# Performance work log

Hardware: AMD Instinct MI355X
Metric: run time of the kernel (lower is better)

## Reference

```python
import jax, jax.numpy as jnp
import numpy as np

N, G, E, R = 32768, 2048, 1146880, 3
NIN, GIN, F, OUT = 6, 4, 64, 1


def _w(k, fan_in, fan_out):
    return (jax.random.normal(k, (fan_in, fan_out), jnp.float32) / np.sqrt(fan_in)).astype(jnp.float32)


def setup_inputs() -> dict:
    key = jax.random.key(0)
    ks = jax.random.split(key, 20)
    x = jax.random.normal(ks[0], (N, NIN), jnp.float32)
    u = jax.random.normal(ks[1], (G, GIN), jnp.float32)
    batch = jnp.sort(jax.random.randint(ks[2], (N,), 0, G))
    hyperedge_index = jax.random.randint(ks[3], (R, E), 0, N)
    batch_hyper = jnp.sort(jax.random.randint(ks[4], (E,), 0, G))
    inp = {
        "x": x, "u": u, "batch": batch,
        "hyperedge_index": hyperedge_index, "batch_hyper": batch_hyper, "r": R,
        # mlp_x: (NIN+GIN)->F->F->F
        "W1": _w(ks[5], NIN + GIN, F), "b1": jnp.zeros((F,), jnp.float32),
        "W2": _w(ks[6], F, F), "b2": jnp.zeros((F,), jnp.float32),
        "W3": _w(ks[7], F, F), "b3": jnp.zeros((F,), jnp.float32),
        # weighting matrix [F,F]
        "weight": _w(ks[8], F, F),
        # x_hat: 2F->F->F->OUT
        "V1": _w(ks[9], 2 * F, F), "c1": jnp.zeros((F,), jnp.float32),
        "V2": _w(ks[10], F, F), "c2": jnp.zeros((F,), jnp.float32),
        "V3": _w(ks[11], F, OUT), "c3": jnp.zeros((OUT,), jnp.float32),
    }
    return inp


def _segment_softmax(x, idx, num_segments):
    # torch_geometric-style softmax grouped by idx along dim 0, per feature
    seg_max = jax.ops.segment_max(x, idx, num_segments=num_segments)
    ex = jnp.exp(x - seg_max[idx])
    denom = jax.ops.segment_sum(ex, idx, num_segments=num_segments)
    return ex / denom[idx]


def reference(x, u, batch, hyperedge_index, batch_hyper, r,
              W1, b1, W2, b2, W3, b3, weight, V1, c1, V2, c2, V3, c3):
    # mlp_x on [node_feats || global_feats_of_node's_graph]
    h = jnp.concatenate([x, u[batch]], axis=1)            # [N, NIN+GIN]
    h = jnp.maximum(h @ W1 + b1, 0.0)
    h = jnp.maximum(h @ W2 + b2, 0.0)
    h = h @ W3 + b3                                        # [N, F]

    # hyperedge finding: sum the r member-node embeddings of each hyperedge
    x_hyper = jnp.zeros((hyperedge_index.shape[1], h.shape[1]), h.dtype)
    for i in range(hyperedge_index.shape[0]):              # r is small & fixed
        x_hyper = x_hyper + jnp.take(h, hyperedge_index[i], axis=0)  # [E, F]

    # weighting: segment softmax over hyperedges of the same graph
    coef = _segment_softmax(x_hyper, batch_hyper, G)       # [E, F]
    x_hyper_hat = coef * jnp.maximum(x_hyper @ weight, 0.0)

    # x_hat head
    o = jnp.concatenate([x_hyper, x_hyper_hat], axis=1)    # [E, 2F]
    o = jnp.maximum(o @ V1 + c1, 0.0)
    o = jnp.maximum(o @ V2 + c2, 0.0)
    o = jax.nn.sigmoid(o @ V3 + c3)                        # [E, OUT]
    return (o, batch_hyper)
```

## Files before the change

### kernel.cpp

```cpp
#include <hip/hip_runtime.h>
#include <math.h>

typedef short bf16x8 __attribute__((ext_vector_type(8)));
typedef float f32x4  __attribute__((ext_vector_type(4)));
typedef unsigned short u16;
typedef unsigned int   u32;

#define MFMA16 __builtin_amdgcn_mfma_f32_16x16x32_bf16

__device__ __forceinline__ u16 f2b(float x) {
    union { float f; unsigned u; } v; v.f = x;
    unsigned r = v.u + 0x7fffu + ((v.u >> 16) & 1u);
    return (u16)(r >> 16);
}
__device__ __forceinline__ u16 f2bu(float x) {
    union { float f; unsigned u; } v; v.f = x;
    return (u16)((v.u + 0x8000u) >> 16);
}
__device__ __forceinline__ float b2f(u16 h) {
    union { unsigned u; float f; } v; v.u = ((unsigned)h) << 16;
    return v.f;
}
__device__ __forceinline__ float blo(u32 w) {
    union { u32 u; float f; } v; v.u = w << 16; return v.f;
}
__device__ __forceinline__ float bhi(u32 w) {
    union { u32 u; float f; } v; v.u = w & 0xffff0000u; return v.f;
}
__device__ __forceinline__ u32 add3pack(u32 x, u32 y, u32 z) {
    union { float f; u32 u; } lo, hi;
    lo.f = blo(x) + blo(y) + blo(z);
    hi.f = bhi(x) + bhi(y) + bhi(z);
    return __builtin_amdgcn_perm(hi.u + 0x8000u, lo.u + 0x8000u, 0x07060302u);
}
__device__ __forceinline__ u32 pack2(float lo, float hi) {
    union { float f; u32 u; } a, b;
    a.f = lo; b.f = hi;
    return __builtin_amdgcn_perm(b.u + 0x8000u, a.u + 0x8000u, 0x07060302u);
}

#define LOG2E 1.44269504088896340736f

__global__ __launch_bounds__(256) void prep_mlp_kernel(
    const float* __restrict__ x, const float* __restrict__ u,
    const int* __restrict__ batch,
    const float* __restrict__ W1, const float* __restrict__ b1,
    const float* __restrict__ W2, const float* __restrict__ b2,
    const float* __restrict__ W3, const float* __restrict__ b3,
    u16* __restrict__ hb, int N,
    const float* __restrict__ Wg, const float* __restrict__ V1g,
    const float* __restrict__ V2g, u16* __restrict__ SWZ,
    const int* __restrict__ bh, int E, int G, int* __restrict__ seg_start,
    int SB)
{
    const int b = blockIdx.x, tid = threadIdx.x;
    if (b < 32) {
        int idx = b * 256 + tid;
        int k = idx >> 6, n = idx & 63;
        int s1 = (k < 64) ? k : (64 + (((k - 64) & 15) << 2) + ((k - 64) >> 4));
        int off1 = ((s1 >> 5) * 4 + (n >> 4)) * 512 + (n & 15) * 32 + ((s1 >> 3) & 3) * 8 + (s1 & 7);
        SWZ[4096 + off1] = f2b(V1g[idx]);
        if (idx < 4096) {
            int offw = ((k >> 5) * 4 + (n >> 4)) * 512 + (n & 15) * 32 + ((k >> 3) & 3) * 8 + (k & 7);
            SWZ[offw] = f2b(Wg[idx]);
            int s2 = ((k & 15) << 2) + (k >> 4);
            int off2 = ((s2 >> 5) * 4 + (n >> 4)) * 512 + (n & 15) * 32 + ((s2 >> 3) & 3) * 8 + (s2 & 7);
            SWZ[12288 + off2] = f2b(V2g[idx]);
        }
        return;
    }
    if (b < 32 + SB) {
        int g = (b - 32) * 256 + tid;
        if (g > G) return;
        int lo = 0, hi = E;
        while (lo < hi) {
            int mid = (lo + hi) >> 1;
            if (bh[mid] < g) lo = mid + 1; else hi = mid;
        }
        seg_start[g] = lo;
        return;
    }
    __shared__ float inbuf[16][10];
    __shared__ float h1[16][64];
    __shared__ float h2[16][64];
    const int ni = tid >> 6, f = tid & 63;
    const int base = (b - 32 - SB) * 16;
    int nodes[4];
    #pragma unroll
    for (int s = 0; s < 4; ++s) {
        nodes[s] = min(base + s * 4 + ni, N - 1);
        if (f < 6)       inbuf[s * 4 + ni][f] = x[nodes[s] * 6 + f];
        else if (f < 10) inbuf[s * 4 + ni][f] = u[batch[nodes[s]] * 4 + (f - 6)];
    }
    __syncthreads();
    float acc[4];
    #pragma unroll
    for (int s = 0; s < 4; ++s) acc[s] = b1[f];
    #pragma unroll
    for (int k = 0; k < 10; ++k) {
        float w = W1[k * 64 + f];
        #pragma unroll
        for (int s = 0; s < 4; ++s) acc[s] = fmaf(inbuf[s * 4 + ni][k], w, acc[s]);
    }
    #pragma unroll
    for (int s = 0; s < 4; ++s) h1[s * 4 + ni][f] = fmaxf(acc[s], 0.f);
    __syncthreads();
    #pragma unroll
    for (int s = 0; s < 4; ++s) acc[s] = b2[f];
    #pragma unroll
    for (int k4 = 0; k4 < 16; ++k4) {
        float w0 = W2[(k4 * 4 + 0) * 64 + f];
        float w1 = W2[(k4 * 4 + 1) * 64 + f];
        float w2 = W2[(k4 * 4 + 2) * 64 + f];
        float w3 = W2[(k4 * 4 + 3) * 64 + f];
        #pragma unroll
        for (int s = 0; s < 4; ++s) {
            float4 hv = *(const float4*)&h1[s * 4 + ni][k4 * 4];
            acc[s] = fmaf(hv.x, w0, acc[s]);
            acc[s] = fmaf(hv.y, w1, acc[s]);
            acc[s] = fmaf(hv.z, w2, acc[s]);
            acc[s] = fmaf(hv.w, w3, acc[s]);
        }
    }
    #pragma unroll
    for (int s = 0; s < 4; ++s) h2[s * 4 + ni][f] = fmaxf(acc[s], 0.f);
    __syncthreads();
    #pragma unroll
    for (int s = 0; s < 4; ++s) acc[s] = b3[f];
    #pragma unroll
    for (int k4 = 0; k4 < 16; ++k4) {
        float w0 = W3[(k4 * 4 + 0) * 64 + f];
        float w1 = W3[(k4 * 4 + 1) * 64 + f];
        float w2 = W3[(k4 * 4 + 2) * 64 + f];
        float w3 = W3[(k4 * 4 + 3) * 64 + f];
        #pragma unroll
        for (int s = 0; s < 4; ++s) {
            float4 hv = *(const float4*)&h2[s * 4 + ni][k4 * 4];
            acc[s] = fmaf(hv.x, w0, acc[s]);
            acc[s] = fmaf(hv.y, w1, acc[s]);
            acc[s] = fmaf(hv.z, w2, acc[s]);
            acc[s] = fmaf(hv.w, w3, acc[s]);
        }
    }
    #pragma unroll
    for (int s = 0; s < 4; ++s) hb[nodes[s] * 64 + f] = f2b(acc[s]);
}

__global__ __launch_bounds__(256) void gather_stats_kernel(
    const u16* __restrict__ hb, const int* __restrict__ hidx,
    const int* __restrict__ seg_start,
    u16* __restrict__ Xh, float* __restrict__ Sinv,
    float* __restrict__ out, int E)
{
    __shared__ float ps[4][8][8];
    const int tid = threadIdx.x, lane = tid & 63, wid = tid >> 6;
    const int sub = lane >> 3, cl = lane & 7;
    const int g = blockIdx.x;
    const int e0 = seg_start[g], e1 = seg_start[g + 1];
    if (e1 <= e0) return;
    const int e1m1 = e1 - 1;
    const float gf = (float)g;

    for (int e = e0 + tid; e < e1; e += 256) out[E + e] = gf;

    float s[8] = {0.f, 0.f, 0.f, 0.f, 0.f, 0.f, 0.f, 0.f};
    for (int e = e0 + wid * 8 + sub; e < e1; e += 128) {
        #pragma unroll
        for (int j = 0; j < 4; ++j) {
            int ee = e + j * 32;
            int ec = min(ee, e1m1);
            int i0 = hidx[ec], i1 = hidx[E + ec], i2 = hidx[2 * E + ec];
            uint4 A0 = *(const uint4*)(hb + (size_t)i0 * 64 + cl * 8);
            uint4 A1 = *(const uint4*)(hb + (size_t)i1 * 64 + cl * 8);
            uint4 A2 = *(const uint4*)(hb + (size_t)i2 * 64 + cl * 8);
            u32 w0 = add3pack(A0.x, A1.x, A2.x);
            u32 w1 = add3pack(A0.y, A1.y, A2.y);
            u32 w2 = add3pack(A0.z, A1.z, A2.z);
            u32 w3 = add3pack(A0.w, A1.w, A2.w);
            if (ee < e1) {
                uint4 W; W.x = w0; W.y = w1; W.z = w2; W.w = w3;
                *(uint4*)(Xh + (size_t)ee * 64 + cl * 8) = W;
                s[0] += __expf(blo(w0)); s[1] += __expf(bhi(w0));
                s[2] += __expf(blo(w1)); s[3] += __expf(bhi(w1));
                s[4] += __expf(blo(w2)); s[5] += __expf(bhi(w2));
                s[6] += __expf(blo(w3)); s[7] += __expf(bhi(w3));
            }
        }
    }
    #pragma unroll
    for (int k = 0; k < 8; ++k) {
        s[k] += __shfl_xor(s[k], 8);
        s[k] += __shfl_xor(s[k], 16);
        s[k] += __shfl_xor(s[k], 32);
    }
    if (lane < 8) {
        #pragma unroll
        for (int k = 0; k < 8; ++k) ps[wid][lane][k] = s[k];
    }
    __syncthreads();
    if (tid < 64) {
        int c8 = tid >> 3, cc = tid & 7;
        float S = ps[0][c8][cc] + ps[1][c8][cc] + ps[2][c8][cc] + ps[3][c8][cc];
        Sinv[g * 64 + tid] = 1.f / S;
    }
}

__global__ __launch_bounds__(256, 4) void mfma_seg_kernel(
    const u16* __restrict__ Xh, const int* __restrict__ seg_start,
    const u16* __restrict__ SWZ, const float* __restrict__ Sinv,
    const float* __restrict__ c1g, const float* __restrict__ c2g,
    const float* __restrict__ V3g, const float* __restrict__ c3g,
    float* __restrict__ out, int E)
{
    __shared__ u16 SW[16384];
    __shared__ u16 XT_all[4][16 * 64];

    const int tid = threadIdx.x, lane = tid & 63, wid = tid >> 6;
    const int nl = lane & 15, rq = lane >> 4;
    const int g = blockIdx.x;
    const int e0 = seg_start[g], e1 = seg_start[g + 1];
    const int L = e1 - e0;
    if (L <= 0) return;
    const int e1m1 = e1 - 1;

    {
        const uint4* src = (const uint4*)SWZ;
        uint4* dst = (uint4*)SW;
        for (int i = tid; i < 2048; i += 256) dst[i] = src[i];
    }
    __syncthreads();
    const u16* WB  = SW;
    const u16* V1B = SW + 4096;
    const u16* V2B = SW + 12288;

    bf16x8 I0, I1;
    #pragma unroll
    for (int j = 0; j < 8; ++j) {
        I0[j] = (rq * 8 + j == nl)      ? (short)0x3F80 : (short)0;
        I1[j] = (rq * 8 + j == nl + 16) ? (short)0x3F80 : (short)0;
    }

    float l2d[4], c1v[4], c2v[4], v3v[4];
    #pragma unroll
    for (int nt = 0; nt < 4; ++nt) {
        int col = nt * 16 + nl;
        l2d[nt] = __log2f(Sinv[g * 64 + col]);
        c1v[nt] = c1g[col];
        c2v[nt] = c2g[col];
        v3v[nt] = V3g[col];
    }
    const float c3s = c3g[0];
    u16* XT = XT_all[wid];
    const f32x4 zf = {0.f, 0.f, 0.f, 0.f};

    const int xw_swz = rq << 4;
    const int xr_base = nl * 64;
    const int xr_swz  = (nl & 12) << 2;
    const int xr0 = xr_base + ((rq * 8) ^ xr_swz);
    const int xr1 = xr_base + ((rq * 8 + 32) ^ xr_swz);

    auto loadA = [&](int tt, bf16x8& A0, bf16x8& A1) {
        const u16* xp = Xh + (size_t)min(e0 + tt * 16 + nl, e1m1) * 64 + rq * 8;
        A0 = *(const bf16x8*)(xp);
        A1 = *(const bf16x8*)(xp + 32);
    };

    int t = wid;
    bf16x8 p0 = {}, p1 = {};
    if (t * 16 < L) loadA(t, p0, p1);

    for (; t * 16 < L; t += 8) {
        const int eB1 = e0 + t * 16;
        const int eB2 = eB1 + 64;

        bf16x8 a0 = p0, a1 = p1;
        bf16x8 a2, a3;
        loadA(t + 4, a2, a3);
        if ((t + 8) * 16 < L) loadA(t + 8, p0, p1);

        f32x4 xc1[4], xc2[4];
        xc1[0] = MFMA16(a0, I0, zf, 0, 0, 0);
        xc1[1] = MFMA16(a0, I1, zf, 0, 0, 0);
        xc1[2] = MFMA16(a1, I0, zf, 0, 0, 0);
        xc1[3] = MFMA16(a1, I1, zf, 0, 0, 0);
        xc2[0] = MFMA16(a2, I0, zf, 0, 0, 0);
        xc2[1] = MFMA16(a2, I1, zf, 0, 0, 0);
        xc2[2] = MFMA16(a3, I0, zf, 0, 0, 0);
        xc2[3] = MFMA16(a3, I1, zf, 0, 0, 0);

        f32x4 acc1[4] = {zf, zf, zf, zf}, acc2t[4] = {zf, zf, zf, zf};
        #pragma unroll
        for (int nt = 0; nt < 4; ++nt) {
            bf16x8 b0 = *(const bf16x8*)(WB + (0 * 4 + nt) * 512 + nl * 32 + rq * 8);
            acc1[nt]  = MFMA16(a0, b0, acc1[nt], 0, 0, 0);
            acc2t[nt] = MFMA16(a2, b0, acc2t[nt], 0, 0, 0);
            bf16x8 b1 = *(const bf16x8*)(WB + (1 * 4 + nt) * 512 + nl * 32 + rq * 8);
            acc1[nt]  = MFMA16(a1, b1, acc1[nt], 0, 0, 0);
            acc2t[nt] = MFMA16(a3, b1, acc2t[nt], 0, 0, 0);
        }
        #pragma unroll
        for (int r = 0; r < 4; ++r) {
            float v0 = __builtin_amdgcn_exp2f(fmaf(xc1[0][r], LOG2E, l2d[0])) * fmaxf(acc1[0][r], 0.f);
            float v1 = __builtin_amdgcn_exp2f(fmaf(xc1[1][r], LOG2E, l2d[1])) * fmaxf(acc1[1][r], 0.f);
            float v2 = __builtin_amdgcn_exp2f(fmaf(xc1[2][r], LOG2E, l2d[2])) * fmaxf(acc1[2][r], 0.f);
            float v3 = __builtin_amdgcn_exp2f(fmaf(xc1[3][r], LOG2E, l2d[3])) * fmaxf(acc1[3][r], 0.f);
            uint2 w; w.x = pack2(v0, v1); w.y = pack2(v2, v3);
            *(uint2*)(XT + (rq * 4 + r) * 64 + ((nl * 4) ^ xw_swz)) = w;
        }
        bf16x8 x2a = *(const bf16x8*)(XT + xr0);
        bf16x8 x3a = *(const bf16x8*)(XT + xr1);
        #pragma unroll
        for (int r = 0; r < 4; ++r) {
            float v0 = __builtin_amdgcn_exp2f(fmaf(xc2[0][r], LOG2E, l2d[0])) * fmaxf(acc2t[0][r], 0.f);
            float v1 = __builtin_amdgcn_exp2f(fmaf(xc2[1][r], LOG2E, l2d[1])) * fmaxf(acc2t[1][r], 0.f);
            float v2 = __builtin_amdgcn_exp2f(fmaf(xc2[2][r], LOG2E, l2d[2])) * fmaxf(acc2t[2][r], 0.f);
            float v3 = __builtin_amdgcn_exp2f(fmaf(xc2[3][r], LOG2E, l2d[3])) * fmaxf(acc2t[3][r], 0.f);
            uint2 w; w.x = pack2(v0, v1); w.y = pack2(v2, v3);
            *(uint2*)(XT + (rq * 4 + r) * 64 + ((nl * 4) ^ xw_swz)) = w;
        }
        bf16x8 x2b = *(const bf16x8*)(XT + xr0);
        bf16x8 x3b = *(const bf16x8*)(XT + xr1);

        f32x4 va[4], vb[4];
        #pragma unroll
        for (int nt = 0; nt < 4; ++nt) {
            va[nt][0] = c1v[nt]; va[nt][1] = c1v[nt];
            va[nt][2] = c1v[nt]; va[nt][3] = c1v[nt];
            vb[nt] = va[nt];
        }
        #pragma unroll
        for (int nt = 0; nt < 4; ++nt) {
            bf16x8 b0 = *(const bf16x8*)(V1B + (0 * 4 + nt) * 512 + nl * 32 + rq * 8);
            va[nt] = MFMA16(a0, b0, va[nt], 0, 0, 0);
            vb[nt] = MFMA16(a2, b0, vb[nt], 0, 0, 0);
            bf16x8 b1 = *(const bf16x8*)(V1B + (1 * 4 + nt) * 512 + nl * 32 + rq * 8);
            va[nt] = MFMA16(a1, b1, va[nt], 0, 0, 0);
            vb[nt] = MFMA16(a3, b1, vb[nt], 0, 0, 0);
        }
        #pragma unroll
        for (int nt = 0; nt < 4; ++nt) {
            bf16x8 b2 = *(const bf16x8*)(V1B + (2 * 4 + nt) * 512 + nl * 32 + rq * 8);
            va[nt] = MFMA16(x2a, b2, va[nt], 0, 0, 0);
            vb[nt] = MFMA16(x2b, b2, vb[nt], 0, 0, 0);
            bf16x8 b3 = *(const bf16x8*)(V1B + (3 * 4 + nt) * 512 + nl * 32 + rq * 8);
            va[nt] = MFMA16(x3a, b3, va[nt], 0, 0, 0);
            vb[nt] = MFMA16(x3b, b3, vb[nt], 0, 0, 0);
        }
        #pragma unroll
        for (int r = 0; r < 4; ++r) {
            uint2 w;
            w.x = pack2(fmaxf(va[0][r], 0.f), fmaxf(va[1][r], 0.f));
            w.y = pack2(fmaxf(va[2][r], 0.f), fmaxf(va[3][r], 0.f));
            *(uint2*)(XT + (rq * 4 + r) * 64 + ((nl * 4) ^ xw_swz)) = w;
        }
        bf16x8 o0a = *(const bf16x8*)(XT + xr0);
        bf16x8 o1a = *(const bf16x8*)(XT + xr1);
        #pragma unroll
        for (int r = 0; r < 4; ++r) {
            uint2 w;
            w.x = pack2(fmaxf(vb[0][r], 0.f), fmaxf(vb[1][r], 0.f));
            w.y = pack2(fmaxf(vb[2][r], 0.f), fmaxf(vb[3][r], 0.f));
            *(uint2*)(XT + (rq * 4 + r) * 64 + ((nl * 4) ^ xw_swz)) = w;
        }
        bf16x8 o0b = *(const bf16x8*)(XT + xr0);
        bf16x8 o1b = *(const bf16x8*)(XT + xr1);

        f32x4 wa[4], wb2[4];
        #pragma unroll
        for (int nt = 0; nt < 4; ++nt) {
            wa[nt][0] = c2v[nt]; wa[nt][1] = c2v[nt];
            wa[nt][2] = c2v[nt]; wa[nt][3] = c2v[nt];
            wb2[nt] = wa[nt];
        }
        #pragma unroll
        for (int nt = 0; nt < 4; ++nt) {
            bf16x8 b0 = *(const bf16x8*)(V2B + (0 * 4 + nt) * 512 + nl * 32 + rq * 8);
            wa[nt]  = MFMA16(o0a, b0, wa[nt], 0, 0, 0);
            wb2[nt] = MFMA16(o0b, b0, wb2[nt], 0, 0, 0);
            bf16x8 b1 = *(const bf16x8*)(V2B + (1 * 4 + nt) * 512 + nl * 32 + rq * 8);
            wa[nt]  = MFMA16(o1a, b1, wa[nt], 0, 0, 0);
            wb2[nt] = MFMA16(o1b, b1, wb2[nt], 0, 0, 0);
        }

        float sra[4], srb[4];
        #pragma unroll
        for (int r = 0; r < 4; ++r) {
            float u1 = 0.f, u2 = 0.f;
            #pragma unroll
            for (int nt = 0; nt < 4; ++nt) {
                u1 = fmaf(fmaxf(wa[nt][r],  0.f), v3v[nt], u1);
                u2 = fmaf(fmaxf(wb2[nt][r], 0.f), v3v[nt], u2);
            }
            u1 += __shfl_xor(u1, 1); u2 += __shfl_xor(u2, 1);
            u1 += __shfl_xor(u1, 2); u2 += __shfl_xor(u2, 2);
            u1 += __shfl_xor(u1, 4); u2 += __shfl_xor(u2, 4);
            u1 += __shfl_xor(u1, 8); u2 += __shfl_xor(u2, 8);
            sra[r] = 1.f / (1.f + __expf(-(u1 + c3s)));
            srb[r] = 1.f / (1.f + __expf(-(u2 + c3s)));
        }
        if (nl == 0) {
            const int ra = eB1 + rq * 4;
            if (ra + 3 < e1) {
                *(float4*)(out + ra) = make_float4(sra[0], sra[1], sra[2], sra[3]);
            } else {
                #pragma unroll
                for (int r = 0; r < 4; ++r)
                    if (ra + r < e1) out[ra + r] = sra[r];
            }
            const int rb = eB2 + rq * 4;
            if (rb + 3 < e1) {
                *(float4*)(out + rb) = make_float4(srb[0], srb[1], srb[2], srb[3]);
            } else {
                #pragma unroll
                for (int r = 0; r < 4; ++r)
                    if (rb + r < e1) out[rb + r] = srb[r];
            }
        }
    }
}

extern "C" void kernel_launch(void* const* d_in, const int* in_sizes, int n_in,
                              void* d_out, int out_size, void* d_ws, size_t ws_size,
                              hipStream_t stream) {
    const float* x     = (const float*)d_in[0];
    const float* u     = (const float*)d_in[1];
    const int*   batch = (const int*)  d_in[2];
    const int*   hidx  = (const int*)  d_in[3];
    const int*   bh    = (const int*)  d_in[4];
    const float* W1 = (const float*)d_in[6];
    const float* b1 = (const float*)d_in[7];
    const float* W2 = (const float*)d_in[8];
    const float* b2 = (const float*)d_in[9];
    const float* W3 = (const float*)d_in[10];
    const float* b3 = (const float*)d_in[11];
    const float* Wg = (const float*)d_in[12];
    const float* V1 = (const float*)d_in[13];
    const float* c1 = (const float*)d_in[14];
    const float* V2 = (const float*)d_in[15];
    const float* c2 = (const float*)d_in[16];
    const float* V3 = (const float*)d_in[17];
    const float* c3 = (const float*)d_in[18];

    const int N = in_sizes[0] / 6;
    const int G = in_sizes[1] / 4;
    const int E = in_sizes[4];

    char* ws = (char*)d_ws;
    size_t off = 0;
    u16* hb = (u16*)(ws + off);            off += (size_t)N * 64 * 2;
    int* seg_start = (int*)(ws + off);     off += ((size_t)G + 1) * 4;
    off = (off + 255) & ~(size_t)255;
    u16* SWZ = (u16*)(ws + off);           off += 16384 * 2;
    float* Sinv = (float*)(ws + off);      off += (size_t)G * 64 * 4;
    off = (off + 255) & ~(size_t)255;
    u16* Xh = (u16*)(ws + off);            off += (size_t)E * 64 * 2;
    float* out = (float*)d_out;

    const int SB = (G + 256) / 256;
    const int NB = (N + 15) / 16;
    prep_mlp_kernel<<<32 + SB + NB, 256, 0, stream>>>(
        x, u, batch, W1, b1, W2, b2, W3, b3, hb, N,
        Wg, V1, V2, SWZ, bh, E, G, seg_start, SB);
    gather_stats_kernel<<<G, 256, 0, stream>>>(hb, hidx, seg_start, Xh, Sinv, out, E);
    mfma_seg_kernel<<<G, 256, 0, stream>>>(
        Xh, seg_start, SWZ, Sinv, c1, c2, V3, c3, out, E);
}
```

Before: 244.3 us.

## Recompute hyperedge sums in MFMA kernel instead of materializing Xh

Removes the E×64 bf16 intermediate buffer Xh that the stats kernel wrote and the MFMA kernel read back. The MFMA kernel now regathers the three member-node rows from hb (which is small and likely cache-resident) and sums them inline. This saves about 147MB of write plus read traffic at the cost of a second random gather, extra index loads and higher register pressure. Occupancy in launch bounds is lowered from 4 to 3 to make room for those registers.

```diff
diff --git a/kernel.cpp b/kernel.cpp
--- a/kernel.cpp
+++ b/kernel.cpp
@@ -149,8 +149,7 @@
 __global__ __launch_bounds__(256) void gather_stats_kernel(
     const u16* __restrict__ hb, const int* __restrict__ hidx,
     const int* __restrict__ seg_start,
-    u16* __restrict__ Xh, float* __restrict__ Sinv,
-    float* __restrict__ out, int E)
+    float* __restrict__ Sinv, float* __restrict__ out, int E)
 {
     __shared__ float ps[4][8][8];
     const int tid = threadIdx.x, lane = tid & 63, wid = tid >> 6;
@@ -178,8 +177,6 @@
             u32 w2 = add3pack(A0.z, A1.z, A2.z);
             u32 w3 = add3pack(A0.w, A1.w, A2.w);
             if (ee < e1) {
-                uint4 W; W.x = w0; W.y = w1; W.z = w2; W.w = w3;
-                *(uint4*)(Xh + (size_t)ee * 64 + cl * 8) = W;
                 s[0] += __expf(blo(w0)); s[1] += __expf(bhi(w0));
                 s[2] += __expf(blo(w1)); s[3] += __expf(bhi(w1));
                 s[4] += __expf(blo(w2)); s[5] += __expf(bhi(w2));
@@ -205,8 +202,9 @@
     }
 }
 
-__global__ __launch_bounds__(256, 4) void mfma_seg_kernel(
-    const u16* __restrict__ Xh, const int* __restrict__ seg_start,
+__global__ __launch_bounds__(256, 3) void mfma_seg_kernel(
+    const u16* __restrict__ hb, const int* __restrict__ hidx,
+    const int* __restrict__ seg_start,
     const u16* __restrict__ SWZ, const float* __restrict__ Sinv,
     const float* __restrict__ c1g, const float* __restrict__ c2g,
     const float* __restrict__ V3g, const float* __restrict__ c3g,
@@ -260,9 +258,25 @@
     const int xr1 = xr_base + ((rq * 8 + 32) ^ xr_swz);
 
     auto loadA = [&](int tt, bf16x8& A0, bf16x8& A1) {
-        const u16* xp = Xh + (size_t)min(e0 + tt * 16 + nl, e1m1) * 64 + rq * 8;
-        A0 = *(const bf16x8*)(xp);
-        A1 = *(const bf16x8*)(xp + 32);
+        const int ec = min(e0 + tt * 16 + nl, e1m1);
+        const int i0 = hidx[ec], i1 = hidx[E + ec], i2 = hidx[2 * E + ec];
+        const u16* r0 = hb + (size_t)i0 * 64 + rq * 8;
+        const u16* r1 = hb + (size_t)i1 * 64 + rq * 8;
+        const u16* r2 = hb + (size_t)i2 * 64 + rq * 8;
+        uint4 B0 = *(const uint4*)(r0), C0 = *(const uint4*)(r0 + 32);
+        uint4 B1 = *(const uint4*)(r1), C1 = *(const uint4*)(r1 + 32);
+        uint4 B2 = *(const uint4*)(r2), C2 = *(const uint4*)(r2 + 32);
+        union { uint4 q; bf16x8 h; } u0, u1v;
+        u0.q.x  = add3pack(B0.x, B1.x, B2.x);
+        u0.q.y  = add3pack(B0.y, B1.y, B2.y);
+        u0.q.z  = add3pack(B0.z, B1.z, B2.z);
+        u0.q.w  = add3pack(B0.w, B1.w, B2.w);
+        u1v.q.x = add3pack(C0.x, C1.x, C2.x);
+        u1v.q.y = add3pack(C0.y, C1.y, C2.y);
+        u1v.q.z = add3pack(C0.z, C1.z, C2.z);
+        u1v.q.w = add3pack(C0.w, C1.w, C2.w);
+        A0 = u0.h;
+        A1 = u1v.h;
     };
 
     int t = wid;
@@ -452,8 +466,6 @@
     off = (off + 255) & ~(size_t)255;
     u16* SWZ = (u16*)(ws + off);           off += 16384 * 2;
     float* Sinv = (float*)(ws + off);      off += (size_t)G * 64 * 4;
-    off = (off + 255) & ~(size_t)255;
-    u16* Xh = (u16*)(ws + off);            off += (size_t)E * 64 * 2;
     float* out = (float*)d_out;
 
     const int SB = (G + 256) / 256;
@@ -461,7 +473,7 @@
     prep_mlp_kernel<<<32 + SB + NB, 256, 0, stream>>>(
         x, u, batch, W1, b1, W2, b2, W3, b3, hb, N,
         Wg, V1, V2, SWZ, bh, E, G, seg_start, SB);
-    gather_stats_kernel<<<G, 256, 0, stream>>>(hb, hidx, seg_start, Xh, Sinv, out, E);
+    gather_stats_kernel<<<G, 256, 0, stream>>>(hb, hidx, seg_start, Sinv, out, E);
     mfma_seg_kernel<<<G, 256, 0, stream>>>(
-        Xh, seg_start, SWZ, Sinv, c1, c2, V3, c3, out, E);
-}
+        hb, hidx, seg_start, SWZ, Sinv, c1, c2, V3, c3, out, E);
+}
```

Result: faster. 238.2 us (-2.5%).
